# Kernel optimization log

Measured on AMD Instinct MI355X. Metric: run time of the kernel, lower is better.

Reference implementation:

```python
import jax, jax.numpy as jnp
import numpy as np
from jax import lax

NEG = -1e30  # finite stand-in for -inf so logaddexp grads stay finite


def setup_inputs() -> dict:
    key = jax.random.key(0)
    k1, k2, k3, k4, k5 = jax.random.split(key, 5)
    B, T, L, S = 16, 2048, 256, 8
    return {
        "emissions": jax.random.normal(k1, (B, T, S), dtype=jnp.float32),
        "transition": jax.random.normal(k2, (S, S), dtype=jnp.float32),
        "bos": jax.random.normal(k3, (S,), dtype=jnp.float32),
        "eos": jax.random.normal(k4, (S,), dtype=jnp.float32),
        "lengths": jnp.full((B,), T, dtype=jnp.int32),
        "targets": jax.random.randint(k5, (B, L), 0, 4, dtype=jnp.int32),
        "target_lengths": jnp.full((B,), L, dtype=jnp.int32),
    }


def _den_logz(em, lengths, transition, bos, eos):
    # Exact log-semiring forward over the fully-connected 8-state denominator CRF graph
    # (the limit of k2.intersect_dense_pruned(...).get_tot_scores(log_semiring=True)).
    B, T, S = em.shape
    alpha0 = bos[None, :] + em[:, 0, :]  # (B,S)

    def step(alpha, em_t):
        a = jax.nn.logsumexp(alpha[:, :, None] + transition[None, :, :], axis=1) + em_t
        return a, a

    _, alphas = lax.scan(step, alpha0, jnp.swapaxes(em, 0, 1)[1:])  # (T-1,B,S)
    alphas = jnp.concatenate([alpha0[None], alphas], axis=0)  # (T,B,S)
    fin = alphas[lengths - 1, jnp.arange(B)]  # (B,S) alpha at last valid frame
    return jax.nn.logsumexp(fin + eos[None, :], axis=-1)


def _num_logz(em, lengths, targets, target_lengths, transition, bos, eos):
    # Forward over the target-constrained enter/extend lattice: symbol u must be
    # entered (state targets[u]) exactly once, optionally extended (state targets[u]+4),
    # then the path moves monotonically to symbol u+1.
    B, T, S = em.shape
    L = targets.shape[1]
    b_idx = jnp.arange(B)
    es = targets          # enter-state ids, (B,L)
    xs = targets + 4      # extend-state ids, (B,L)

    t_xx = transition[xs, xs]  # extend_u -> extend_u
    t_ex = transition[es, xs]  # enter_u  -> extend_u
    prev_e = jnp.concatenate([es[:, :1], es[:, :-1]], axis=1)
    prev_x = jnp.concatenate([xs[:, :1], xs[:, :-1]], axis=1)
    t_ee = transition[prev_e, es]  # enter_{u-1}  -> enter_u
    t_xe = transition[prev_x, es]  # extend_{u-1} -> enter_u

    a_e0 = jnp.full((B, L), NEG, dtype=em.dtype)
    a_e0 = a_e0.at[:, 0].set(bos[es[:, 0]] + em[b_idx, 0, es[:, 0]])
    a_x0 = jnp.full((B, L), NEG, dtype=em.dtype)

    def shift(a):  # a[:, u-1], NEG at u=0
        return jnp.concatenate([jnp.full((B, 1), NEG, dtype=a.dtype), a[:, :-1]], axis=1)

    def step(carry, em_t):
        a_e, a_x = carry
        em_e = jnp.take_along_axis(em_t, es, axis=1)  # (B,L)
        em_x = jnp.take_along_axis(em_t, xs, axis=1)
        new_e = em_e + jnp.logaddexp(shift(a_e) + t_ee, shift(a_x) + t_xe)
        new_x = em_x + jnp.logaddexp(a_e + t_ex, a_x + t_xx)
        return (new_e, new_x), (new_e, new_x)

    _, (ae, ax) = lax.scan(step, (a_e0, a_x0), jnp.swapaxes(em, 0, 1)[1:])
    ae = jnp.concatenate([a_e0[None], ae], axis=0)  # (T,B,L)
    ax = jnp.concatenate([a_x0[None], ax], axis=0)
    fin_e = ae[lengths - 1, b_idx]  # (B,L)
    fin_x = ax[lengths - 1, b_idx]
    u = target_lengths - 1
    fe = fin_e[b_idx, u] + eos[es[b_idx, u]]
    fx = fin_x[b_idx, u] + eos[xs[b_idx, u]]
    return jnp.logaddexp(fe, fx)  # (B,)


def reference(emissions, transition, bos, eos, lengths, targets, target_lengths):
    em = emissions.astype(jnp.float32)
    logz_den = _den_logz(em, lengths, transition, bos, eos)
    logz_num = _num_logz(em, lengths, targets, target_lengths, transition, bos, eos)
    # all samples valid by construction (lengths > 0, 0 < target_len <= length)
    return jnp.mean(logz_den - logz_num)
```

## Files before the change

### kernel.cpp

```cpp
#include <hip/hip_runtime.h>
#include <math.h>


#define LOG2E 1.4426950408889634f
#define LN2   0.69314718055994531f
#define CTL_WSHL1  0x130
#define CTL_WSHR1  0x138
#define CTL_ROR(r) (0x120 + (r))

#define AST(p, v) __hip_atomic_store((p), (v), __ATOMIC_RELAXED, __HIP_MEMORY_SCOPE_AGENT)
#define ALD(p)    __hip_atomic_load((p), __ATOMIC_RELAXED, __HIP_MEMORY_SCOPE_AGENT)

template <int CTRL>
__device__ __forceinline__ float fdpp(float x) {
    return __int_as_float(__builtin_amdgcn_update_dpp(
        0, __float_as_int(x), CTRL, 0xF, 0xF, true));
}
template <int CTRL>
__device__ __forceinline__ int idpp(int x) {
    return __builtin_amdgcn_update_dpp(0, x, CTRL, 0xF, 0xF, true);
}

__device__ __forceinline__ void pin() {
#if __has_builtin(__builtin_amdgcn_sched_barrier)
    __builtin_amdgcn_sched_barrier(0);
#else
    asm volatile("" ::: "memory");
#endif
}

__device__ __forceinline__ float fexp2(float x) {
#if __has_builtin(__builtin_amdgcn_exp2f)
    return __builtin_amdgcn_exp2f(x);
#else
    return exp2f(x);
#endif
}
__device__ __forceinline__ float flog2(float x) {
#if __has_builtin(__builtin_amdgcn_logf)
    return __builtin_amdgcn_logf(x);
#else
    return __log2f(x);
#endif
}
__device__ __forceinline__ float lse2(float a, float b) {
    float m = fmaxf(a, b);
    float d = fminf(a, b) - m;
    return m + flog2(1.0f + fexp2(d));
}

struct NumC { float tee[4], txe[4], tex[4], txx[4]; };

__device__ __forceinline__ void numf_step(const float2* p, float* E, float* X,
                                          float teeF, float txeF, const NumC& c) {
    float nbE = fdpp<CTL_WSHR1>(E[3]);
    float nbX = fdpp<CTL_WSHR1>(X[3]);
    float nE0 = p[0].x * fmaf(nbE,  teeF,     nbX  * txeF);
    float nE1 = p[1].x * fmaf(E[0], c.tee[1], X[0] * c.txe[1]);
    float nE2 = p[2].x * fmaf(E[1], c.tee[2], X[1] * c.txe[2]);
    float nE3 = p[3].x * fmaf(E[2], c.tee[3], X[2] * c.txe[3]);
    float nX0 = p[0].y * fmaf(E[0], c.tex[0], X[0] * c.txx[0]);
    float nX1 = p[1].y * fmaf(E[1], c.tex[1], X[1] * c.txx[1]);
    float nX2 = p[2].y * fmaf(E[2], c.tex[2], X[2] * c.txx[2]);
    float nX3 = p[3].y * fmaf(E[3], c.tex[3], X[3] * c.txx[3]);
    E[0] = nE0; E[1] = nE1; E[2] = nE2; E[3] = nE3;
    X[0] = nX0; X[1] = nX1; X[2] = nX2; X[3] = nX3;
}

__device__ __forceinline__ void numf_boundary(float* E, float* X, int& s,
                                              float& teeF, float& txeF,
                                              int lane, const NumC& c) {
    float m = fmaxf(fmaxf(fmaxf(E[0], E[1]), fmaxf(E[2], E[3])),
                    fmaxf(fmaxf(X[0], X[1]), fmaxf(X[2], X[3])));
    const bool live = (m > 0.0f);
    const int ex = live ? ((int)(__float_as_uint(m) >> 23) - 126) : 0;
    s += ex;
    const int bs = idpp<CTL_WSHR1>(s);
    if (!live) s = bs;
    int d = (lane == 0) ? 0 : (bs - s);
    const int extra = (d > 30) ? d : 0;
    s += extra; d -= extra;
    const float fsc = ldexpf(1.0f, -(ex + extra));
#pragma unroll
    for (int k = 0; k < 4; ++k) { E[k] *= fsc; X[k] *= fsc; }
    const float fs0 = (lane == 0) ? 0.0f : ldexpf(1.0f, d);
    teeF = c.tee[0] * fs0;
    txeF = c.txe[0] * fs0;
}

__device__ __forceinline__ void numb_step(const float2* p, float* bE, float* bX,
                                          const float* tex, const float* txx,
                                          const float* teeN, const float* txeN,
                                          float teeN3F, float txeN3F) {
    float mm0 = p[0].x * bE[0];
    float mm1 = p[1].x * bE[1];
    float mm2 = p[2].x * bE[2];
    float mm3 = p[3].x * bE[3];
    float m10 = p[0].y * bX[0];
    float m11 = p[1].y * bX[1];
    float m12 = p[2].y * bX[2];
    float m13 = p[3].y * bX[3];
    float mup = fdpp<CTL_WSHL1>(mm0);
    float nE0 = fmaf(tex[0], m10, teeN[0] * mm1);
    float nE1 = fmaf(tex[1], m11, teeN[1] * mm2);
    float nE2 = fmaf(tex[2], m12, teeN[2] * mm3);
    float nE3 = fmaf(tex[3], m13, teeN3F   * mup);
    float nX0 = fmaf(txx[0], m10, txeN[0] * mm1);
    float nX1 = fmaf(txx[1], m11, txeN[1] * mm2);
    float nX2 = fmaf(txx[2], m12, txeN[2] * mm3);
    float nX3 = fmaf(txx[3], m13, txeN3F   * mup);
    bE[0] = nE0; bE[1] = nE1; bE[2] = nE2; bE[3] = nE3;
    bX[0] = nX0; bX[1] = nX1; bX[2] = nX2; bX[3] = nX3;
}

__device__ __forceinline__ void numb_boundary(float* bE, float* bX, int& s,
                                              float& teeN3F, float& txeN3F,
                                              int lane, float teeN3, float txeN3) {
    float m = fmaxf(fmaxf(fmaxf(bE[0], bE[1]), fmaxf(bE[2], bE[3])),
                    fmaxf(fmaxf(bX[0], bX[1]), fmaxf(bX[2], bX[3])));
    const bool live = (m > 0.0f);
    const int ex = live ? ((int)(__float_as_uint(m) >> 23) - 126) : 0;
    s += ex;
    const int bs = idpp<CTL_WSHL1>(s);
    if (!live) s = bs;
    int d = (lane == 63) ? 0 : (bs - s);
    const int extra = (d > 30) ? d : 0;
    s += extra; d -= extra;
    const float fsc = ldexpf(1.0f, -(ex + extra));
#pragma unroll
    for (int k = 0; k < 4; ++k) { bE[k] *= fsc; bX[k] *= fsc; }
    const float fs = (lane == 63) ? 0.0f : ldexpf(1.0f, d);
    teeN3F = teeN3 * fs;
    txeN3F = txeN3 * fs;
}

__device__ __forceinline__ void steps4_fwd(const float4 buf[4][2], float* E, float* X,
                                           float teeF, float txeF, const NumC& c) {
#pragma unroll
    for (int q = 0; q < 4; ++q) {
        float2 p[4];
#pragma unroll
        for (int k = 0; k < 4; ++k) {
            const float4 v = buf[k][q >> 1];
            p[k] = (q & 1) ? make_float2(v.z, v.w) : make_float2(v.x, v.y);
        }
        numf_step(p, E, X, teeF, txeF, c);
    }
}
__device__ __forceinline__ void steps4_bwd(const float4 buf[4][2], float* bE, float* bX,
                                           const float* tex, const float* txx,
                                           const float* teeN, const float* txeN,
                                           float teeN3F, float txeN3F) {
#pragma unroll
    for (int q = 0; q < 4; ++q) {
        const int h = 1 - (q >> 1);
        float2 p[4];
#pragma unroll
        for (int k = 0; k < 4; ++k) {
            const float4 v = buf[k][h];
            p[k] = (q & 1) ? make_float2(v.x, v.y) : make_float2(v.z, v.w);
        }
        numb_step(p, bE, bX, tex, txx, teeN, txeN, teeN3F, txeN3F);
    }
}

__device__ __forceinline__ float denf_step(float al, float emt, const float* Tr) {
    float v1 = fdpp<CTL_ROR(1)>(al);
    float v2 = fdpp<CTL_ROR(2)>(al);
    float v3 = fdpp<CTL_ROR(3)>(al);
    float v4 = fdpp<CTL_ROR(4)>(al);
    float v5 = fdpp<CTL_ROR(5)>(al);
    float v6 = fdpp<CTL_ROR(6)>(al);
    float v7 = fdpp<CTL_ROR(7)>(al);
    float q0 = fmaf(v1, Tr[1], al * Tr[0]);
    float q1 = fmaf(v3, Tr[3], v2 * Tr[2]);
    float q2 = fmaf(v5, Tr[5], v4 * Tr[4]);
    float q3 = fmaf(v7, Tr[7], v6 * Tr[6]);
    return ((q0 + q1) + (q2 + q3)) * emt;
}
__device__ __forceinline__ float denb_step(float al, float emt, const float* TrB) {
    float g  = al * emt;
    float v1 = fdpp<CTL_ROR(7)>(g);
    float v2 = fdpp<CTL_ROR(6)>(g);
    float v3 = fdpp<CTL_ROR(5)>(g);
    float v4 = fdpp<CTL_ROR(4)>(g);
    float v5 = fdpp<CTL_ROR(3)>(g);
    float v6 = fdpp<CTL_ROR(2)>(g);
    float v7 = fdpp<CTL_ROR(1)>(g);
    float q0 = fmaf(v1, TrB[1], g * TrB[0]);
    float q1 = fmaf(v3, TrB[3], v2 * TrB[2]);
    float q2 = fmaf(v5, TrB[5], v4 * TrB[4]);
    float q3 = fmaf(v7, TrB[7], v6 * TrB[6]);
    return (q0 + q1) + (q2 + q3);
}
__device__ __forceinline__ int den_renorm(float& al) {
    float mm = fmaxf(al, fdpp<CTL_ROR(4)>(al));
    mm = fmaxf(mm, fdpp<CTL_ROR(2)>(mm));
    mm = fmaxf(mm, fdpp<CTL_ROR(1)>(mm));
    const int ex = (int)(__float_as_uint(mm) >> 23) - 126;
    al = ldexpf(al, -ex);
    return ex;
}

extern "C" __global__ void __launch_bounds__(128)
crf_fused(const float* __restrict__ em, const float* __restrict__ trans,
          const float* __restrict__ bos, const float* __restrict__ eos,
          const int* __restrict__ lengths, const int* __restrict__ targets,
          const int* __restrict__ tlens,
          float* __restrict__ ws, float* __restrict__ out,
          int B, int T, int S, int L)
{
    extern __shared__ float sm[];
    const int bid  = blockIdx.x;
    const int tid  = threadIdx.x;
    const int lane = tid & 63;
    const int wv   = tid >> 6;
    const int half = S >> 1;
    const int role = bid / B;
    const int b    = bid % B;
    const float* gem = em + (size_t)b * T * S;
    const int len = lengths[b];
    const int tm  = (len - 1) >> 1;
    const int P2  = T + 2;
    const int Th2 = P2 >> 1;

    float* NF  = ws + 16 + (size_t)b * 576;
    float* NB  = ws + 16 + (size_t)B * 576 + (size_t)b * 576;
    float* DEN = ws + 16 + (size_t)(2 * B) * 576;
    int* ticket = (int*)ws;

    if (role < 2) {
        float2* s2 = (float2*)sm;
        for (int t = tid; t < T; t += 128) {
            const float4* gr = (const float4*)(gem + t * S);
            float4 a = gr[0], c4 = gr[1];
            s2[0 * P2 + t] = make_float2(fexp2(a.x * LOG2E), fexp2(c4.x * LOG2E));
            s2[1 * P2 + t] = make_float2(fexp2(a.y * LOG2E), fexp2(c4.y * LOG2E));
            s2[2 * P2 + t] = make_float2(fexp2(a.z * LOG2E), fexp2(c4.z * LOG2E));
            s2[3 * P2 + t] = make_float2(fexp2(a.w * LOG2E), fexp2(c4.w * LOG2E));
        }
    } else {
        for (int t = tid; t < T; t += 128) {
            const float4* gr = (const float4*)(gem + t * S);
            float4 a = gr[0], c4 = gr[1];
            float4 w0, w1;
            w0.x = fexp2(a.x * LOG2E); w0.y = fexp2(c4.x * LOG2E);
            w0.z = fexp2(a.y * LOG2E); w0.w = fexp2(c4.y * LOG2E);
            w1.x = fexp2(a.z * LOG2E); w1.y = fexp2(c4.z * LOG2E);
            w1.z = fexp2(a.w * LOG2E); w1.w = fexp2(c4.w * LOG2E);
            ((float4*)sm)[t * 2]     = w0;
            ((float4*)sm)[t * 2 + 1] = w1;
        }
    }
    __syncthreads();

    if (role == 0 && wv == 0) {
        const float2* s2 = (const float2*)sm;
        const float4* s4 = (const float4*)sm;
        const int u0 = lane * 4;
        int e[4], ep[4];
        const int base = b * L;
#pragma unroll
        for (int k = 0; k < 4; ++k) {
            int u = u0 + k;
            e[k] = targets[base + ((u < L) ? u : (L - 1))];
        }
        ep[0] = (u0 > 0) ? targets[base + u0 - 1] : e[0];
        ep[1] = e[0]; ep[2] = e[1]; ep[3] = e[2];
        NumC c;
#pragma unroll
        for (int k = 0; k < 4; ++k) {
            c.tee[k] = fexp2(trans[ep[k] * S + e[k]] * LOG2E);
            c.txe[k] = fexp2(trans[(ep[k] + half) * S + e[k]] * LOG2E);
            c.tex[k] = fexp2(trans[e[k] * S + e[k] + half] * LOG2E);
            c.txx[k] = fexp2(trans[(e[k] + half) * S + e[k] + half] * LOG2E);
        }
        float E[4] = {0.f,0.f,0.f,0.f}, X[4] = {0.f,0.f,0.f,0.f};
        int s = 0;
        if (lane == 0) E[0] = fexp2(bos[e[0]] * LOG2E) * s2[e[0] * P2].x;
        float teeF = (lane == 0) ? 0.0f : c.tee[0];
        float txeF = (lane == 0) ? 0.0f : c.txe[0];

        int t0 = 1;
        while (t0 <= tm && (t0 & 1)) {
            float2 p[4];
#pragma unroll
            for (int k = 0; k < 4; ++k) p[k] = s2[e[k] * P2 + t0];
            numf_step(p, E, X, teeF, txeF, c);
            ++t0;
        }
        if (t0 + 7 <= tm) {
            float4 A[4][2], Bf[4][2];
#pragma unroll
            for (int k = 0; k < 4; ++k) {
                A[k][0] = s4[e[k] * Th2 + (t0 >> 1)];
                A[k][1] = s4[e[k] * Th2 + ((t0 + 2) >> 1)];
            }
            pin();
            while (t0 + 7 <= tm) {
#pragma unroll
                for (int k = 0; k < 4; ++k) {
                    Bf[k][0] = s4[e[k] * Th2 + ((t0 + 4) >> 1)];
                    Bf[k][1] = s4[e[k] * Th2 + ((t0 + 6) >> 1)];
                }
                pin();
                steps4_fwd(A, E, X, teeF, txeF, c);
#pragma unroll
                for (int k = 0; k < 4; ++k) {
                    A[k][0] = s4[e[k] * Th2 + ((t0 + 8) >> 1)];
                    A[k][1] = s4[e[k] * Th2 + ((t0 + 10) >> 1)];
                }
                pin();
                steps4_fwd(Bf, E, X, teeF, txeF, c);
                numf_boundary(E, X, s, teeF, txeF, lane, c);
                t0 += 8;
            }
        }
        while (t0 <= tm) {
            float2 p[4];
#pragma unroll
            for (int k = 0; k < 4; ++k) p[k] = s2[e[k] * P2 + t0];
            numf_step(p, E, X, teeF, txeF, c);
            ++t0;
        }
#pragma unroll
        for (int k = 0; k < 4; ++k) {
            AST(&NF[lane * 8 + k],     E[k]);
            AST(&NF[lane * 8 + 4 + k], X[k]);
        }
        AST(&NF[512 + lane], __int_as_float(s));
    } else if (role == 1 && wv == 0) {
        const float2* s2 = (const float2*)sm;
        const float4* s4 = (const float4*)sm;
        const int u0 = lane * 4;
        int e[5];
        const int base = b * L;
#pragma unroll
        for (int k = 0; k < 5; ++k) {
            int u = u0 + k;
            e[k] = targets[base + ((u < L) ? u : (L - 1))];
        }
        float tex[4], txx[4], teeN[4], txeN[4];
#pragma unroll
        for (int k = 0; k < 4; ++k) {
            tex[k]  = fexp2(trans[e[k] * S + e[k] + half] * LOG2E);
            txx[k]  = fexp2(trans[(e[k] + half) * S + e[k] + half] * LOG2E);
            teeN[k] = fexp2(trans[e[k] * S + e[k + 1]] * LOG2E);
            txeN[k] = fexp2(trans[(e[k] + half) * S + e[k + 1]] * LOG2E);
        }
        if (lane == 63) { teeN[3] = 0.0f; txeN[3] = 0.0f; }
        float bE[4] = {0.f,0.f,0.f,0.f}, bX[4] = {0.f,0.f,0.f,0.f};
        const int uf = tlens[b] - 1;
        if (lane == (uf >> 2)) {
            const int kf = uf & 3;
            bE[kf] = fexp2(eos[e[kf]] * LOG2E);
            bX[kf] = fexp2(eos[e[kf] + half] * LOG2E);
        }
        int s = 0;
        float teeN3F = teeN[3], txeN3F = txeN[3];

        int t1 = len - 1;
        const int tlo = tm + 1;
        while (t1 >= tlo && !(t1 & 1)) {
            float2 p[4];
#pragma unroll
            for (int k = 0; k < 4; ++k) p[k] = s2[e[k] * P2 + t1];
            numb_step(p, bE, bX, tex, txx, teeN, txeN, teeN3F, txeN3F);
            --t1;
        }
        if (t1 - 7 >= tlo) {
            float4 A[4][2], Bf[4][2];
#pragma unroll
            for (int k = 0; k < 4; ++k) {
                A[k][0] = s4[e[k] * Th2 + ((t1 - 3) >> 1)];
                A[k][1] = s4[e[k] * Th2 + ((t1 - 1) >> 1)];
            }
            pin();
            while (t1 - 7 >= tlo) {
#pragma unroll
                for (int k = 0; k < 4; ++k) {
                    Bf[k][0] = s4[e[k] * Th2 + ((t1 - 7) >> 1)];
                    Bf[k][1] = s4[e[k] * Th2 + ((t1 - 5) >> 1)];
                }
                pin();
                steps4_bwd(A, bE, bX, tex, txx, teeN, txeN, teeN3F, txeN3F);
                const int ta = (t1 - 11 > 0) ? (t1 - 11) : 0;
#pragma unroll
                for (int k = 0; k < 4; ++k) {
                    A[k][0] = s4[e[k] * Th2 + (ta >> 1)];
                    A[k][1] = s4[e[k] * Th2 + ((ta + 2) >> 1)];
                }
                pin();
                steps4_bwd(Bf, bE, bX, tex, txx, teeN, txeN, teeN3F, txeN3F);
                numb_boundary(bE, bX, s, teeN3F, txeN3F, lane, teeN[3], txeN[3]);
                t1 -= 8;
            }
        }
        while (t1 >= tlo) {
            float2 p[4];
#pragma unroll
            for (int k = 0; k < 4; ++k) p[k] = s2[e[k] * P2 + t1];
            numb_step(p, bE, bX, tex, txx, teeN, txeN, teeN3F, txeN3F);
            --t1;
        }
#pragma unroll
        for (int k = 0; k < 4; ++k) {
            AST(&NB[lane * 8 + k],     bE[k]);
            AST(&NB[lane * 8 + 4 + k], bX[k]);
        }
        AST(&NB[512 + lane], __int_as_float(s));
    } else if (role == 2) {
        float* denF  = sm + T * 8 + 16;
        float* denB  = denF + 8;
        int*   denFs = (int*)(denB + 8);
        int*   denBs = denFs + 8;
        const int j  = lane & 7;
        const int jj = ((j & 3) << 1) + (j >> 2);
        if (wv == 0) {
            float Tr[8];
#pragma unroll
            for (int r = 0; r < 8; ++r)
                Tr[r] = fexp2(trans[((j - r) & 7) * S + j] * LOG2E);
            float al = fexp2(bos[j] * LOG2E) * sm[jj];
            int sc = 0;
            int t = 1;
            while (t + 3 <= tm) {
                float c0 = sm[t * 8 + jj];
                float c1 = sm[(t + 1) * 8 + jj];
                float c2 = sm[(t + 2) * 8 + jj];
                float c3 = sm[(t + 3) * 8 + jj];
                pin();
                al = denf_step(al, c0, Tr);
                al = denf_step(al, c1, Tr);
                al = denf_step(al, c2, Tr);
                al = denf_step(al, c3, Tr);
                sc += den_renorm(al);
                t += 4;
            }
            while (t <= tm) { al = denf_step(al, sm[t * 8 + jj], Tr); ++t; }
            if (lane < 8) { denF[j] = al; denFs[j] = sc; }
        } else {
            float TrB[8];
#pragma unroll
            for (int r = 0; r < 8; ++r)
                TrB[r] = fexp2(trans[j * S + ((j + r) & 7)] * LOG2E);
            float al = fexp2(eos[j] * LOG2E);
            int sc = 0;
            int t = len - 1;
            const int tlo = tm + 1;
            while (t - 3 >= tlo) {
                float c0 = sm[t * 8 + jj];
                float c1 = sm[(t - 1) * 8 + jj];
                float c2 = sm[(t - 2) * 8 + jj];
                float c3 = sm[(t - 3) * 8 + jj];
                pin();
                al = denb_step(al, c0, TrB);
                al = denb_step(al, c1, TrB);
                al = denb_step(al, c2, TrB);
                al = denb_step(al, c3, TrB);
                sc += den_renorm(al);
                t -= 4;
            }
            while (t >= tlo) { al = denb_step(al, sm[t * 8 + jj], TrB); --t; }
            if (lane < 8) { denB[j] = al; denBs[j] = sc; }
        }
        __syncthreads();
        if (wv == 0 && lane < 8) {
            const float a  = fmaxf(denF[j], 1e-37f);
            const float bb = fmaxf(denB[j], 1e-37f);
            float part = flog2(a) + flog2(bb) + (float)(denFs[j] + denBs[j]);
            part = lse2(part, __shfl_xor(part, 1, 64));
            part = lse2(part, __shfl_xor(part, 2, 64));
            part = lse2(part, __shfl_xor(part, 4, 64));
            if (j == 0) AST(&DEN[b], part);
        }
    }

    __syncthreads();
    int* wflag = (int*)sm;
    if (tid == 0) {
        __threadfence();
        const int tk = atomicAdd(ticket, 1);
        wflag[0] = (tk == 3 * B - 1) ? 1 : 0;
    }
    __syncthreads();
    if (wflag[0] && tid < 64) {
        __threadfence();
        float acc = 0.0f;
        for (int bb2 = 0; bb2 < B; ++bb2) {
            const float* nf = ws + 16 + (size_t)bb2 * 576;
            const float* nb = ws + 16 + (size_t)B * 576 + (size_t)bb2 * 576;
            float v = 0.0f;
#pragma unroll
            for (int k = 0; k < 8; ++k)
                v = fmaf(ALD(&nf[lane * 8 + k]), ALD(&nb[lane * 8 + k]), v);
            const int st = __float_as_int(ALD(&nf[512 + lane]))
                         + __float_as_int(ALD(&nb[512 + lane]));
            float part = (v > 0.0f) ? (flog2(v) + (float)st) : -3.0e38f;
#pragma unroll
            for (int o = 1; o < 64; o <<= 1)
                part = lse2(part, __shfl_xor(part, o, 64));
            if (lane == 0) acc += ALD(&DEN[bb2]) - part;
        }
        if (lane == 0) out[0] = acc * (LN2 / (float)B);
    }
}

extern "C" void kernel_launch(void* const* d_in, const int* in_sizes, int n_in,
                              void* d_out, int out_size, void* d_ws, size_t ws_size,
                              hipStream_t stream)
{
    const float* em      = (const float*)d_in[0];
    const float* trans   = (const float*)d_in[1];
    const float* bos     = (const float*)d_in[2];
    const float* eos     = (const float*)d_in[3];
    const int*   lengths = (const int*)d_in[4];
    const int*   targets = (const int*)d_in[5];
    const int*   tlens   = (const int*)d_in[6];
    float* out = (float*)d_out;
    float* ws  = (float*)d_ws;

    const int B  = in_sizes[4];
    const int SS = in_sizes[1];
    int S = 1; while (S * S < SS) ++S;
    const int T = in_sizes[0] / (B * S);
    const int L = in_sizes[5] / B;

    const size_t shmem = (size_t)(T * 8 + 80) * sizeof(float);

    (void)hipMemsetAsync(ws, 0, 64, stream);
    hipLaunchKernelGGL(crf_fused, dim3(3 * B), dim3(128), shmem, stream,
                       em, trans, bos, eos, lengths, targets, tlens,
                       ws, out, B, T, S, L);
}
```

Measured before the change: 159.7 us.

## Split numerator lattice across two waves with LDS ring-buffer wavefront pipeline

The numerator forward and backward recursions previously ran on a single wave, with 4 lattice symbols per lane. They now use both waves of the block, each lane owning 2 symbols. The two waves run skewed by one 16-step chunk and pass the boundary lane's state and scale exponent through a double-buffered LDS ring, with a block barrier per chunk. This halves the per-step serial arithmetic per lane but adds LDS traffic and __syncthreads on the critical path. The denominator loops also gain software-prefetched emission loads for the next 4-step group.

```diff
diff --git a/kernel.cpp b/kernel.cpp
--- a/kernel.cpp
+++ b/kernel.cpp
@@ -49,118 +49,112 @@
     return m + flog2(1.0f + fexp2(d));
 }
 
-struct NumC { float tee[4], txe[4], tex[4], txx[4]; };
-
-__device__ __forceinline__ void numf_step(const float2* p, float* E, float* X,
-                                          float teeF, float txeF, const NumC& c) {
-    float nbE = fdpp<CTL_WSHR1>(E[3]);
-    float nbX = fdpp<CTL_WSHR1>(X[3]);
-    float nE0 = p[0].x * fmaf(nbE,  teeF,     nbX  * txeF);
-    float nE1 = p[1].x * fmaf(E[0], c.tee[1], X[0] * c.txe[1]);
-    float nE2 = p[2].x * fmaf(E[1], c.tee[2], X[1] * c.txe[2]);
-    float nE3 = p[3].x * fmaf(E[2], c.tee[3], X[2] * c.txe[3]);
-    float nX0 = p[0].y * fmaf(E[0], c.tex[0], X[0] * c.txx[0]);
-    float nX1 = p[1].y * fmaf(E[1], c.tex[1], X[1] * c.txx[1]);
-    float nX2 = p[2].y * fmaf(E[2], c.tex[2], X[2] * c.txx[2]);
-    float nX3 = p[3].y * fmaf(E[3], c.tex[3], X[3] * c.txx[3]);
-    E[0] = nE0; E[1] = nE1; E[2] = nE2; E[3] = nE3;
-    X[0] = nX0; X[1] = nX1; X[2] = nX2; X[3] = nX3;
-}
-
-__device__ __forceinline__ void numf_boundary(float* E, float* X, int& s,
-                                              float& teeF, float& txeF,
-                                              int lane, const NumC& c) {
-    float m = fmaxf(fmaxf(fmaxf(E[0], E[1]), fmaxf(E[2], E[3])),
-                    fmaxf(fmaxf(X[0], X[1]), fmaxf(X[2], X[3])));
-    const bool live = (m > 0.0f);
-    const int ex = live ? ((int)(__float_as_uint(m) >> 23) - 126) : 0;
-    s += ex;
-    const int bs = idpp<CTL_WSHR1>(s);
-    if (!live) s = bs;
-    int d = (lane == 0) ? 0 : (bs - s);
-    const int extra = (d > 30) ? d : 0;
-    s += extra; d -= extra;
-    const float fsc = ldexpf(1.0f, -(ex + extra));
-#pragma unroll
-    for (int k = 0; k < 4; ++k) { E[k] *= fsc; X[k] *= fsc; }
-    const float fs0 = (lane == 0) ? 0.0f : ldexpf(1.0f, d);
-    teeF = c.tee[0] * fs0;
-    txeF = c.txe[0] * fs0;
-}
-
-__device__ __forceinline__ void numb_step(const float2* p, float* bE, float* bX,
-                                          const float* tex, const float* txx,
-                                          const float* teeN, const float* txeN,
-                                          float teeN3F, float txeN3F) {
-    float mm0 = p[0].x * bE[0];
-    float mm1 = p[1].x * bE[1];
-    float mm2 = p[2].x * bE[2];
-    float mm3 = p[3].x * bE[3];
-    float m10 = p[0].y * bX[0];
-    float m11 = p[1].y * bX[1];
-    float m12 = p[2].y * bX[2];
-    float m13 = p[3].y * bX[3];
-    float mup = fdpp<CTL_WSHL1>(mm0);
-    float nE0 = fmaf(tex[0], m10, teeN[0] * mm1);
-    float nE1 = fmaf(tex[1], m11, teeN[1] * mm2);
-    float nE2 = fmaf(tex[2], m12, teeN[2] * mm3);
-    float nE3 = fmaf(tex[3], m13, teeN3F   * mup);
-    float nX0 = fmaf(txx[0], m10, txeN[0] * mm1);
-    float nX1 = fmaf(txx[1], m11, txeN[1] * mm2);
-    float nX2 = fmaf(txx[2], m12, txeN[2] * mm3);
-    float nX3 = fmaf(txx[3], m13, txeN3F   * mup);
-    bE[0] = nE0; bE[1] = nE1; bE[2] = nE2; bE[3] = nE3;
-    bX[0] = nX0; bX[1] = nX1; bX[2] = nX2; bX[3] = nX3;
-}
-
-__device__ __forceinline__ void numb_boundary(float* bE, float* bX, int& s,
-                                              float& teeN3F, float& txeN3F,
-                                              int lane, float teeN3, float txeN3) {
-    float m = fmaxf(fmaxf(fmaxf(bE[0], bE[1]), fmaxf(bE[2], bE[3])),
-                    fmaxf(fmaxf(bX[0], bX[1]), fmaxf(bX[2], bX[3])));
-    const bool live = (m > 0.0f);
-    const int ex = live ? ((int)(__float_as_uint(m) >> 23) - 126) : 0;
-    s += ex;
-    const int bs = idpp<CTL_WSHL1>(s);
-    if (!live) s = bs;
-    int d = (lane == 63) ? 0 : (bs - s);
-    const int extra = (d > 30) ? d : 0;
-    s += extra; d -= extra;
-    const float fsc = ldexpf(1.0f, -(ex + extra));
-#pragma unroll
-    for (int k = 0; k < 4; ++k) { bE[k] *= fsc; bX[k] *= fsc; }
-    const float fs = (lane == 63) ? 0.0f : ldexpf(1.0f, d);
-    teeN3F = teeN3 * fs;
-    txeN3F = txeN3 * fs;
-}
-
-__device__ __forceinline__ void steps4_fwd(const float4 buf[4][2], float* E, float* X,
-                                           float teeF, float txeF, const NumC& c) {
-#pragma unroll
-    for (int q = 0; q < 4; ++q) {
-        float2 p[4];
-#pragma unroll
-        for (int k = 0; k < 4; ++k) {
-            const float4 v = buf[k][q >> 1];
-            p[k] = (q & 1) ? make_float2(v.z, v.w) : make_float2(v.x, v.y);
-        }
-        numf_step(p, E, X, teeF, txeF, c);
-    }
-}
-__device__ __forceinline__ void steps4_bwd(const float4 buf[4][2], float* bE, float* bX,
-                                           const float* tex, const float* txx,
-                                           const float* teeN, const float* txeN,
-                                           float teeN3F, float txeN3F) {
-#pragma unroll
-    for (int q = 0; q < 4; ++q) {
-        const int h = 1 - (q >> 1);
-        float2 p[4];
-#pragma unroll
-        for (int k = 0; k < 4; ++k) {
-            const float4 v = buf[k][h];
-            p[k] = (q & 1) ? make_float2(v.x, v.y) : make_float2(v.z, v.w);
-        }
-        numb_step(p, bE, bX, tex, txx, teeN, txeN, teeN3F, txeN3F);
+#define NFW_STEP {                                                          \
+    float2 q0 = st0[tb + k + 1], q1 = st1[tb + k + 1];                      \
+    float2 rv = make_float2(0.0f, 0.0f);                                    \
+    if (CONS) rv = rEX[k * 64 + 63];                                        \
+    float nbE = fdpp<CTL_WSHR1>(E[1]);                                      \
+    float nbX = fdpp<CTL_WSHR1>(X[1]);                                      \
+    if (CONS && l0) { nbE = rv.x; nbX = rv.y; }                             \
+    float nE0 = p0.x * fmaf(nbE,  teeF, nbX  * txeF);                       \
+    float nE1 = p1.x * fmaf(E[0], tee1, X[0] * txe1);                       \
+    float nX0 = p0.y * fmaf(E[0], tex0, X[0] * txx0);                       \
+    float nX1 = p1.y * fmaf(E[1], tex1, X[1] * txx1);                       \
+    E[0] = nE0; E[1] = nE1; X[0] = nX0; X[1] = nX1;                         \
+    if (!CONS) rEX[(k + 1) * 64 + lane] = make_float2(E[1], X[1]);          \
+    if ((k & 7) == 7) {                                                     \
+        int rs = 0;                                                         \
+        if (CONS) rs = rS[(k >> 3) * 64 + 63];                              \
+        float m = fmaxf(fmaxf(E[0], E[1]), fmaxf(X[0], X[1]));              \
+        const bool live = (m > 0.0f);                                       \
+        const int ex = live ? ((int)(__float_as_uint(m) >> 23) - 126) : 0;  \
+        s += ex;                                                            \
+        int bs = idpp<CTL_WSHR1>(s);                                        \
+        if (CONS && l0) bs = rs;                                            \
+        if (!live) s = bs;                                                  \
+        int d = (g == 0) ? 0 : (bs - s);                                    \
+        const int extra = (d > 30) ? d : 0;                                 \
+        s += extra; d -= extra;                                             \
+        const float fsc = ldexpf(1.0f, -(ex + extra));                      \
+        E[0] *= fsc; E[1] *= fsc; X[0] *= fsc; X[1] *= fsc;                 \
+        const float fs0 = (g == 0) ? 0.0f : ldexpf(1.0f, d);                \
+        teeF = tee0 * fs0; txeF = txe0 * fs0;                               \
+        if (!CONS) { rS[(k >> 3) * 64 + lane] = s;                          \
+                     rEX[(k + 1) * 64 + lane] = make_float2(E[1], X[1]); }  \
+    }                                                                       \
+    p0 = q0; p1 = q1; }
+
+template <bool CONS>
+__device__ __forceinline__ void nfwd_chunk(
+    const float2* st0, const float2* st1,
+    float (&E)[2], float (&X)[2], int& s, float& teeF, float& txeF,
+    float tee0, float txe0, float tee1, float txe1,
+    float tex0, float txx0, float tex1, float txx1,
+    int tb, int n, int g, int lane, float2* rEX, int* rS)
+{
+    const bool l0 = (lane == 0);
+    if (!CONS) rEX[lane] = make_float2(E[1], X[1]);
+    float2 p0 = st0[tb], p1 = st1[tb];
+    if (n == 16) {
+#pragma unroll
+        for (int k = 0; k < 16; ++k) NFW_STEP
+    } else {
+        for (int k = 0; k < n; ++k) NFW_STEP
+    }
+}
+
+#define NBW_STEP {                                                          \
+    float2 q0 = st0[tb - k - 1], q1 = st1[tb - k - 1];                      \
+    float rm = 0.0f;                                                        \
+    if (CONS) rm = rM[k * 64];                                              \
+    float mm0 = p0.x * bE[0];                                               \
+    float mm1 = p1.x * bE[1];                                               \
+    float m10 = p0.y * bX[0];                                               \
+    float m11 = p1.y * bX[1];                                               \
+    float mup = fdpp<CTL_WSHL1>(mm0);                                       \
+    if (CONS && l63) mup = rm;                                              \
+    if (!CONS) rM[k * 64 + lane] = mm0;                                     \
+    float nE0 = fmaf(tex0, m10, teeN0 * mm1);                               \
+    float nX0 = fmaf(txx0, m10, txeN0 * mm1);                               \
+    float nE1 = fmaf(tex1, m11, teeN1F * mup);                              \
+    float nX1 = fmaf(txx1, m11, txeN1F * mup);                              \
+    bE[0] = nE0; bE[1] = nE1; bX[0] = nX0; bX[1] = nX1;                     \
+    if ((k & 7) == 7) {                                                     \
+        int rs = 0;                                                         \
+        if (CONS) rs = rS[(k >> 3) * 64];                                   \
+        float m = fmaxf(fmaxf(bE[0], bE[1]), fmaxf(bX[0], bX[1]));          \
+        const bool live = (m > 0.0f);                                       \
+        const int ex = live ? ((int)(__float_as_uint(m) >> 23) - 126) : 0;  \
+        s += ex;                                                            \
+        int bs = idpp<CTL_WSHL1>(s);                                        \
+        if (CONS && l63) bs = rs;                                           \
+        if (!live) s = bs;                                                  \
+        int d = (g == 127) ? 0 : (bs - s);                                  \
+        const int extra = (d > 30) ? d : 0;                                 \
+        s += extra; d -= extra;                                             \
+        const float fsc = ldexpf(1.0f, -(ex + extra));                      \
+        bE[0] *= fsc; bE[1] *= fsc; bX[0] *= fsc; bX[1] *= fsc;             \
+        const float fs = (g == 127) ? 0.0f : ldexpf(1.0f, d);               \
+        teeN1F = teeN1 * fs; txeN1F = txeN1 * fs;                           \
+        if (!CONS) rS[(k >> 3) * 64 + lane] = s;                            \
+    }                                                                       \
+    p0 = q0; p1 = q1; }
+
+template <bool CONS>
+__device__ __forceinline__ void nbwd_chunk(
+    const float2* st0, const float2* st1,
+    float (&bE)[2], float (&bX)[2], int& s, float& teeN1F, float& txeN1F,
+    float teeN0, float txeN0, float teeN1, float txeN1,
+    float tex0, float txx0, float tex1, float txx1,
+    int tb, int n, int g, int lane, float* rM, int* rS)
+{
+    const bool l63 = (lane == 63);
+    float2 p0 = st0[tb], p1 = st1[tb];
+    if (n == 16) {
+#pragma unroll
+        for (int k = 0; k < 16; ++k) NBW_STEP
+    } else {
+        for (int k = 0; k < n; ++k) NBW_STEP
     }
 }
 
@@ -222,11 +216,11 @@
     const int len = lengths[b];
     const int tm  = (len - 1) >> 1;
     const int P2  = T + 2;
-    const int Th2 = P2 >> 1;
-
-    float* NF  = ws + 16 + (size_t)b * 576;
-    float* NB  = ws + 16 + (size_t)B * 576 + (size_t)b * 576;
-    float* DEN = ws + 16 + (size_t)(2 * B) * 576;
+    const int RINGF = 8 * P2;
+
+    float* NF  = ws + 16 + (size_t)b * 640;
+    float* NB  = ws + 16 + (size_t)B * 640 + (size_t)b * 640;
+    float* DEN = ws + 16 + (size_t)(2 * B) * 640;
     int* ticket = (int*)ws;
 
     if (role < 2) {
@@ -254,162 +248,119 @@
     }
     __syncthreads();
 
-    if (role == 0 && wv == 0) {
-        const float2* s2 = (const float2*)sm;
-        const float4* s4 = (const float4*)sm;
-        const int u0 = lane * 4;
-        int e[4], ep[4];
+    if (role == 0) {
+        const float2* s2v = (const float2*)sm;
+        const int g   = (wv << 6) + lane;
+        const int u0g = g * 2;
         const int base = b * L;
-#pragma unroll
-        for (int k = 0; k < 4; ++k) {
-            int u = u0 + k;
-            e[k] = targets[base + ((u < L) ? u : (L - 1))];
-        }
-        ep[0] = (u0 > 0) ? targets[base + u0 - 1] : e[0];
-        ep[1] = e[0]; ep[2] = e[1]; ep[3] = e[2];
-        NumC c;
-#pragma unroll
-        for (int k = 0; k < 4; ++k) {
-            c.tee[k] = fexp2(trans[ep[k] * S + e[k]] * LOG2E);
-            c.txe[k] = fexp2(trans[(ep[k] + half) * S + e[k]] * LOG2E);
-            c.tex[k] = fexp2(trans[e[k] * S + e[k] + half] * LOG2E);
-            c.txx[k] = fexp2(trans[(e[k] + half) * S + e[k] + half] * LOG2E);
-        }
-        float E[4] = {0.f,0.f,0.f,0.f}, X[4] = {0.f,0.f,0.f,0.f};
+        const int e0 = targets[base + ((u0g     < L) ? u0g     : (L - 1))];
+        const int e1 = targets[base + ((u0g + 1 < L) ? u0g + 1 : (L - 1))];
+        const int ep = (u0g > 0) ? targets[base + u0g - 1] : e0;
+        const float tee0 = fexp2(trans[ep * S + e0] * LOG2E);
+        const float txe0 = fexp2(trans[(ep + half) * S + e0] * LOG2E);
+        const float tee1 = fexp2(trans[e0 * S + e1] * LOG2E);
+        const float txe1 = fexp2(trans[(e0 + half) * S + e1] * LOG2E);
+        const float tex0 = fexp2(trans[e0 * S + e0 + half] * LOG2E);
+        const float txx0 = fexp2(trans[(e0 + half) * S + e0 + half] * LOG2E);
+        const float tex1 = fexp2(trans[e1 * S + e1 + half] * LOG2E);
+        const float txx1 = fexp2(trans[(e1 + half) * S + e1 + half] * LOG2E);
+        const float2* st0 = s2v + e0 * P2;
+        const float2* st1 = s2v + e1 * P2;
+        float E[2] = {0.f, 0.f}, X[2] = {0.f, 0.f};
         int s = 0;
-        if (lane == 0) E[0] = fexp2(bos[e[0]] * LOG2E) * s2[e[0] * P2].x;
-        float teeF = (lane == 0) ? 0.0f : c.tee[0];
-        float txeF = (lane == 0) ? 0.0f : c.txe[0];
-
-        int t0 = 1;
-        while (t0 <= tm && (t0 & 1)) {
-            float2 p[4];
-#pragma unroll
-            for (int k = 0; k < 4; ++k) p[k] = s2[e[k] * P2 + t0];
-            numf_step(p, E, X, teeF, txeF, c);
-            ++t0;
-        }
-        if (t0 + 7 <= tm) {
-            float4 A[4][2], Bf[4][2];
-#pragma unroll
-            for (int k = 0; k < 4; ++k) {
-                A[k][0] = s4[e[k] * Th2 + (t0 >> 1)];
-                A[k][1] = s4[e[k] * Th2 + ((t0 + 2) >> 1)];
+        if (g == 0) E[0] = fexp2(bos[e0] * LOG2E) * st0[0].x;
+        float teeF = (g == 0) ? 0.0f : tee0;
+        float txeF = (g == 0) ? 0.0f : txe0;
+
+        float2* ringEX = (float2*)(sm + RINGF);
+        int*    ringS  = (int*)(sm + RINGF + 4352);
+        const int NCH = (tm + 15) >> 4;
+        for (int ph = 0; ph <= NCH; ++ph) {
+            const int ci = (wv == 0) ? ph : ph - 1;
+            if (ci >= 0 && ci < NCH) {
+                const int tb = 1 + (ci << 4);
+                int n = tm - tb + 1; if (n > 16) n = 16;
+                float2* rEX = ringEX + (ci & 1) * (17 * 64);
+                int*    rS  = ringS  + (ci & 1) * 128;
+                if (wv == 0)
+                    nfwd_chunk<false>(st0, st1, E, X, s, teeF, txeF,
+                                      tee0, txe0, tee1, txe1,
+                                      tex0, txx0, tex1, txx1,
+                                      tb, n, g, lane, rEX, rS);
+                else
+                    nfwd_chunk<true>(st0, st1, E, X, s, teeF, txeF,
+                                     tee0, txe0, tee1, txe1,
+                                     tex0, txx0, tex1, txx1,
+                                     tb, n, g, lane, rEX, rS);
             }
-            pin();
-            while (t0 + 7 <= tm) {
-#pragma unroll
-                for (int k = 0; k < 4; ++k) {
-                    Bf[k][0] = s4[e[k] * Th2 + ((t0 + 4) >> 1)];
-                    Bf[k][1] = s4[e[k] * Th2 + ((t0 + 6) >> 1)];
-                }
-                pin();
-                steps4_fwd(A, E, X, teeF, txeF, c);
-#pragma unroll
-                for (int k = 0; k < 4; ++k) {
-                    A[k][0] = s4[e[k] * Th2 + ((t0 + 8) >> 1)];
-                    A[k][1] = s4[e[k] * Th2 + ((t0 + 10) >> 1)];
-                }
-                pin();
-                steps4_fwd(Bf, E, X, teeF, txeF, c);
-                numf_boundary(E, X, s, teeF, txeF, lane, c);
-                t0 += 8;
+            __syncthreads();
+        }
+        AST(&NF[g * 4 + 0], E[0]);
+        AST(&NF[g * 4 + 1], E[1]);
+        AST(&NF[g * 4 + 2], X[0]);
+        AST(&NF[g * 4 + 3], X[1]);
+        AST(&NF[512 + g], __int_as_float(s));
+    } else if (role == 1) {
+        const float2* s2v = (const float2*)sm;
+        const int g   = (wv << 6) + lane;
+        const int u0g = g * 2;
+        const int base = b * L;
+        const int e0 = targets[base + ((u0g     < L) ? u0g     : (L - 1))];
+        const int e1 = targets[base + ((u0g + 1 < L) ? u0g + 1 : (L - 1))];
+        const int e2 = targets[base + ((u0g + 2 < L) ? u0g + 2 : (L - 1))];
+        const float tex0 = fexp2(trans[e0 * S + e0 + half] * LOG2E);
+        const float txx0 = fexp2(trans[(e0 + half) * S + e0 + half] * LOG2E);
+        const float tex1 = fexp2(trans[e1 * S + e1 + half] * LOG2E);
+        const float txx1 = fexp2(trans[(e1 + half) * S + e1 + half] * LOG2E);
+        const float teeN0 = fexp2(trans[e0 * S + e1] * LOG2E);
+        const float txeN0 = fexp2(trans[(e0 + half) * S + e1] * LOG2E);
+        float teeN1 = fexp2(trans[e1 * S + e2] * LOG2E);
+        float txeN1 = fexp2(trans[(e1 + half) * S + e2] * LOG2E);
+        if (g == 127) { teeN1 = 0.0f; txeN1 = 0.0f; }
+        const float2* st0 = s2v + e0 * P2;
+        const float2* st1 = s2v + e1 * P2;
+        float bE[2] = {0.f, 0.f}, bX[2] = {0.f, 0.f};
+        const int uf = tlens[b] - 1;
+        if (g == (uf >> 1)) {
+            const int kf = uf & 1;
+            const int ef = kf ? e1 : e0;
+            bE[kf] = fexp2(eos[ef] * LOG2E);
+            bX[kf] = fexp2(eos[ef + half] * LOG2E);
+        }
+        int s = 0;
+        float teeN1F = teeN1, txeN1F = txeN1;
+
+        float* ringM = sm + RINGF;
+        int*   ringS = (int*)(sm + RINGF + 4352);
+        const int th = len - 1, tlo = tm + 1;
+        const int nbs = th - tlo + 1;
+        const int NCH = (nbs > 0) ? ((nbs + 15) >> 4) : 0;
+        for (int ph = 0; ph <= NCH; ++ph) {
+            const int ci = (wv == 1) ? ph : ph - 1;
+            if (ci >= 0 && ci < NCH) {
+                const int tb = th - (ci << 4);
+                int n = tb - tlo + 1; if (n > 16) n = 16;
+                float* rM = ringM + (ci & 1) * 1024;
+                int*   rS = ringS + (ci & 1) * 128;
+                if (wv == 1)
+                    nbwd_chunk<false>(st0, st1, bE, bX, s, teeN1F, txeN1F,
+                                      teeN0, txeN0, teeN1, txeN1,
+                                      tex0, txx0, tex1, txx1,
+                                      tb, n, g, lane, rM, rS);
+                else
+                    nbwd_chunk<true>(st0, st1, bE, bX, s, teeN1F, txeN1F,
+                                     teeN0, txeN0, teeN1, txeN1,
+                                     tex0, txx0, tex1, txx1,
+                                     tb, n, g, lane, rM, rS);
             }
-        }
-        while (t0 <= tm) {
-            float2 p[4];
-#pragma unroll
-            for (int k = 0; k < 4; ++k) p[k] = s2[e[k] * P2 + t0];
-            numf_step(p, E, X, teeF, txeF, c);
-            ++t0;
-        }
-#pragma unroll
-        for (int k = 0; k < 4; ++k) {
-            AST(&NF[lane * 8 + k],     E[k]);
-            AST(&NF[lane * 8 + 4 + k], X[k]);
-        }
-        AST(&NF[512 + lane], __int_as_float(s));
-    } else if (role == 1 && wv == 0) {
-        const float2* s2 = (const float2*)sm;
-        const float4* s4 = (const float4*)sm;
-        const int u0 = lane * 4;
-        int e[5];
-        const int base = b * L;
-#pragma unroll
-        for (int k = 0; k < 5; ++k) {
-            int u = u0 + k;
-            e[k] = targets[base + ((u < L) ? u : (L - 1))];
-        }
-        float tex[4], txx[4], teeN[4], txeN[4];
-#pragma unroll
-        for (int k = 0; k < 4; ++k) {
-            tex[k]  = fexp2(trans[e[k] * S + e[k] + half] * LOG2E);
-            txx[k]  = fexp2(trans[(e[k] + half) * S + e[k] + half] * LOG2E);
-            teeN[k] = fexp2(trans[e[k] * S + e[k + 1]] * LOG2E);
-            txeN[k] = fexp2(trans[(e[k] + half) * S + e[k + 1]] * LOG2E);
-        }
-        if (lane == 63) { teeN[3] = 0.0f; txeN[3] = 0.0f; }
-        float bE[4] = {0.f,0.f,0.f,0.f}, bX[4] = {0.f,0.f,0.f,0.f};
-        const int uf = tlens[b] - 1;
-        if (lane == (uf >> 2)) {
-            const int kf = uf & 3;
-            bE[kf] = fexp2(eos[e[kf]] * LOG2E);
-            bX[kf] = fexp2(eos[e[kf] + half] * LOG2E);
-        }
-        int s = 0;
-        float teeN3F = teeN[3], txeN3F = txeN[3];
-
-        int t1 = len - 1;
-        const int tlo = tm + 1;
-        while (t1 >= tlo && !(t1 & 1)) {
-            float2 p[4];
-#pragma unroll
-            for (int k = 0; k < 4; ++k) p[k] = s2[e[k] * P2 + t1];
-            numb_step(p, bE, bX, tex, txx, teeN, txeN, teeN3F, txeN3F);
-            --t1;
-        }
-        if (t1 - 7 >= tlo) {
-            float4 A[4][2], Bf[4][2];
-#pragma unroll
-            for (int k = 0; k < 4; ++k) {
-                A[k][0] = s4[e[k] * Th2 + ((t1 - 3) >> 1)];
-                A[k][1] = s4[e[k] * Th2 + ((t1 - 1) >> 1)];
-            }
-            pin();
-            while (t1 - 7 >= tlo) {
-#pragma unroll
-                for (int k = 0; k < 4; ++k) {
-                    Bf[k][0] = s4[e[k] * Th2 + ((t1 - 7) >> 1)];
-                    Bf[k][1] = s4[e[k] * Th2 + ((t1 - 5) >> 1)];
-                }
-                pin();
-                steps4_bwd(A, bE, bX, tex, txx, teeN, txeN, teeN3F, txeN3F);
-                const int ta = (t1 - 11 > 0) ? (t1 - 11) : 0;
-#pragma unroll
-                for (int k = 0; k < 4; ++k) {
-                    A[k][0] = s4[e[k] * Th2 + (ta >> 1)];
-                    A[k][1] = s4[e[k] * Th2 + ((ta + 2) >> 1)];
-                }
-                pin();
-                steps4_bwd(Bf, bE, bX, tex, txx, teeN, txeN, teeN3F, txeN3F);
-                numb_boundary(bE, bX, s, teeN3F, txeN3F, lane, teeN[3], txeN[3]);
-                t1 -= 8;
-            }
-        }
-        while (t1 >= tlo) {
-            float2 p[4];
-#pragma unroll
-            for (int k = 0; k < 4; ++k) p[k] = s2[e[k] * P2 + t1];
-            numb_step(p, bE, bX, tex, txx, teeN, txeN, teeN3F, txeN3F);
-            --t1;
-        }
-#pragma unroll
-        for (int k = 0; k < 4; ++k) {
-            AST(&NB[lane * 8 + k],     bE[k]);
-            AST(&NB[lane * 8 + 4 + k], bX[k]);
-        }
-        AST(&NB[512 + lane], __int_as_float(s));
-    } else if (role == 2) {
+            __syncthreads();
+        }
+        AST(&NB[g * 4 + 0], bE[0]);
+        AST(&NB[g * 4 + 1], bE[1]);
+        AST(&NB[g * 4 + 2], bX[0]);
+        AST(&NB[g * 4 + 3], bX[1]);
+        AST(&NB[512 + g], __int_as_float(s));
+    } else {
         float* denF  = sm + T * 8 + 16;
         float* denB  = denF + 8;
         int*   denFs = (int*)(denB + 8);
@@ -424,12 +375,26 @@
             float al = fexp2(bos[j] * LOG2E) * sm[jj];
             int sc = 0;
             int t = 1;
-            while (t + 3 <= tm) {
+            if (t + 3 <= tm) {
                 float c0 = sm[t * 8 + jj];
                 float c1 = sm[(t + 1) * 8 + jj];
                 float c2 = sm[(t + 2) * 8 + jj];
                 float c3 = sm[(t + 3) * 8 + jj];
                 pin();
+                while (t + 7 <= tm) {
+                    float d0 = sm[(t + 4) * 8 + jj];
+                    float d1 = sm[(t + 5) * 8 + jj];
+                    float d2 = sm[(t + 6) * 8 + jj];
+                    float d3 = sm[(t + 7) * 8 + jj];
+                    pin();
+                    al = denf_step(al, c0, Tr);
+                    al = denf_step(al, c1, Tr);
+                    al = denf_step(al, c2, Tr);
+                    al = denf_step(al, c3, Tr);
+                    sc += den_renorm(al);
+                    c0 = d0; c1 = d1; c2 = d2; c3 = d3;
+                    t += 4;
+                }
                 al = denf_step(al, c0, Tr);
                 al = denf_step(al, c1, Tr);
                 al = denf_step(al, c2, Tr);
@@ -448,12 +413,26 @@
             int sc = 0;
             int t = len - 1;
             const int tlo = tm + 1;
-            while (t - 3 >= tlo) {
+            if (t - 3 >= tlo) {
                 float c0 = sm[t * 8 + jj];
                 float c1 = sm[(t - 1) * 8 + jj];
                 float c2 = sm[(t - 2) * 8 + jj];
                 float c3 = sm[(t - 3) * 8 + jj];
                 pin();
+                while (t - 7 >= tlo) {
+                    float d0 = sm[(t - 4) * 8 + jj];
+                    float d1 = sm[(t - 5) * 8 + jj];
+                    float d2 = sm[(t - 6) * 8 + jj];
+                    float d3 = sm[(t - 7) * 8 + jj];
+                    pin();
+                    al = denb_step(al, c0, TrB);
+                    al = denb_step(al, c1, TrB);
+                    al = denb_step(al, c2, TrB);
+                    al = denb_step(al, c3, TrB);
+                    sc += den_renorm(al);
+                    c0 = d0; c1 = d1; c2 = d2; c3 = d3;
+                    t -= 4;
+                }
                 al = denb_step(al, c0, TrB);
                 al = denb_step(al, c1, TrB);
                 al = denb_step(al, c2, TrB);
@@ -488,15 +467,23 @@
         __threadfence();
         float acc = 0.0f;
         for (int bb2 = 0; bb2 < B; ++bb2) {
-            const float* nf = ws + 16 + (size_t)bb2 * 576;
-            const float* nb = ws + 16 + (size_t)B * 576 + (size_t)bb2 * 576;
-            float v = 0.0f;
-#pragma unroll
-            for (int k = 0; k < 8; ++k)
-                v = fmaf(ALD(&nf[lane * 8 + k]), ALD(&nb[lane * 8 + k]), v);
-            const int st = __float_as_int(ALD(&nf[512 + lane]))
+            const float* nf = ws + 16 + (size_t)bb2 * 640;
+            const float* nb = ws + 16 + (size_t)B * 640 + (size_t)bb2 * 640;
+            float va = 0.0f, vb = 0.0f;
+#pragma unroll
+            for (int k = 0; k < 4; ++k)
+                va = fmaf(ALD(&nf[lane * 4 + k]), ALD(&nb[lane * 4 + k]), va);
+#pragma unroll
+            for (int k = 0; k < 4; ++k)
+                vb = fmaf(ALD(&nf[256 + lane * 4 + k]),
+                          ALD(&nb[256 + lane * 4 + k]), vb);
+            const int sa = __float_as_int(ALD(&nf[512 + lane]))
                          + __float_as_int(ALD(&nb[512 + lane]));
-            float part = (v > 0.0f) ? (flog2(v) + (float)st) : -3.0e38f;
+            const int sb = __float_as_int(ALD(&nf[576 + lane]))
+                         + __float_as_int(ALD(&nb[576 + lane]));
+            float pa = (va > 0.0f) ? (flog2(va) + (float)sa) : -3.0e38f;
+            float pb = (vb > 0.0f) ? (flog2(vb) + (float)sb) : -3.0e38f;
+            float part = lse2(pa, pb);
 #pragma unroll
             for (int o = 1; o < 64; o <<= 1)
                 part = lse2(part, __shfl_xor(part, o, 64));
@@ -526,7 +513,15 @@
     const int T = in_sizes[0] / (B * S);
     const int L = in_sizes[5] / B;
 
-    const size_t shmem = (size_t)(T * 8 + 80) * sizeof(float);
+    const size_t shmem = (size_t)(8 * (T + 2) + 4352 + 256) * sizeof(float);
+
+    static bool attr_done = false;
+    if (!attr_done) {
+        (void)hipFuncSetAttribute((const void*)crf_fused,
+                                  hipFuncAttributeMaxDynamicSharedMemorySize,
+                                  (int)(96 * 1024));
+        attr_done = true;
+    }
 
     (void)hipMemsetAsync(ws, 0, 64, stream);
     hipLaunchKernelGGL(crf_fused, dim3(3 * B), dim3(128), shmem, stream,
```

Measured after the change: 150.8 us. 1.06x faster.
